# Optimization experiments

Hardware: AMD Instinct MI355X
Metric: run time of the kernel (lower is better)

Reference implementation:

```python
import jax, jax.numpy as jnp
import numpy as np

N_NODES = 50000
N_EDGES = 800000
HID = 128
EDGE_DIM = 4
LAYERS = 4
MAX_Z = 100
NUM_GRAPHS = 512


def setup_inputs() -> dict:
    key = jax.random.key(0)
    ks = jax.random.split(key, 16)
    s = lambda k, shape, fan_in: jax.random.normal(k, shape, jnp.float32) / np.sqrt(fan_in)
    inp = {
        "z": jax.random.randint(ks[0], (N_NODES,), 0, MAX_Z + 1),
        "edge_index": jax.random.randint(ks[1], (2, N_EDGES), 0, N_NODES),
        "edge_attr": jax.random.normal(ks[2], (N_EDGES, EDGE_DIM), jnp.float32),
        "batch": jnp.sort(jax.random.randint(ks[3], (N_NODES,), 0, NUM_GRAPHS)),
        "emb": jax.random.normal(ks[4], (MAX_Z + 1, HID), jnp.float32),
        # stacked per-layer params; Linear stored as [in, out]
        "ew1": s(ks[5], (LAYERS, 2 * HID + EDGE_DIM, HID), 2 * HID + EDGE_DIM),
        "eb1": jnp.zeros((LAYERS, HID), jnp.float32),
        "ew2": s(ks[6], (LAYERS, HID, HID), HID),
        "eb2": jnp.zeros((LAYERS, HID), jnp.float32),
        "nw": s(ks[7], (LAYERS, 2 * HID, HID), 2 * HID),
        "nb": jnp.zeros((LAYERS, HID), jnp.float32),
        "rw1": s(ks[8], (HID, HID), HID),
        "rb1": jnp.zeros((HID,), jnp.float32),
        "rw2": s(ks[9], (HID, 1), HID),
        "rb2": jnp.zeros((1,), jnp.float32),
    }
    return inp


def _forward(z, edge_index, edge_attr, batch,
             emb, ew1, eb1, ew2, eb2, nw, nb, rw1, rb1, rw2, rb2):
    silu = jax.nn.silu
    src, dst = edge_index[0], edge_index[1]
    x = emb[z]  # [N, H]
    for l in range(LAYERS):
        m_in = jnp.concatenate([x[src], x[dst], edge_attr], axis=-1)  # [E, 2H+ed]
        h = silu(m_in @ ew1[l] + eb1[l])
        msg = silu(h @ ew2[l] + eb2[l])  # [E, H]
        agg = jax.ops.segment_sum(msg, dst, num_segments=N_NODES)  # scatter-add
        x = silu(jnp.concatenate([x, agg], axis=-1) @ nw[l] + nb[l])
    # segment mean over graphs
    sums = jax.ops.segment_sum(x, batch, num_segments=NUM_GRAPHS)
    counts = jnp.clip(jax.ops.segment_sum(jnp.ones((x.shape[0],), x.dtype), batch,
                                          num_segments=NUM_GRAPHS), 1.0)[:, None]
    g = sums / counts  # [G, H]
    pred = (silu(g @ rw1 + rb1) @ rw2 + rb2)[:, 0]  # [G]
    return pred


def reference(z, edge_index, edge_attr, batch,
              emb, ew1, eb1, ew2, eb2, nw, nb, rw1, rb1, rw2, rb2):
    return _forward(z, edge_index, edge_attr, batch,
                    emb, ew1, eb1, ew2, eb2, nw, nb, rw1, rb1, rw2, rb2)
```

## Files before the change

### kernel.cpp

```cpp
#include <hip/hip_runtime.h>
#include <math.h>

#define HID  128
#define EDIM 4

typedef unsigned short u16;
typedef u16    us8   __attribute__((ext_vector_type(8)));
typedef __bf16 bf16x8 __attribute__((ext_vector_type(8)));
typedef float  f32x4 __attribute__((ext_vector_type(4)));

__device__ __forceinline__ float silu_f(float v) {
    return v * __builtin_amdgcn_rcpf(1.0f + __expf(-v));
}
__device__ __forceinline__ u16 f2bf(float f) {
    unsigned u = __float_as_uint(f);
    unsigned r = u + 0x7fffu + ((u >> 16) & 1u);
    return (u16)(r >> 16);
}
__device__ __forceinline__ u16 f2bf_fast(float f) {
    return (u16)((__float_as_uint(f) + 0x8000u) >> 16);
}
__device__ __forceinline__ float bf2f(u16 s) {
    return __uint_as_float(((unsigned)s) << 16);
}
__device__ __forceinline__ bf16x8 as_bf(us8 v) {
    return __builtin_bit_cast(bf16x8, v);
}

__device__ __forceinline__ void wfrag_one(const float* __restrict__ w,
        u16* __restrict__ out, int KT, int K, int idx) {
    int lane = idx & 63;
    int f    = (idx >> 6) % (KT * 8);
    int l    = idx / (64 * KT * 8);
    int kt = f >> 3, nt = f & 7;
    int n  = nt * 16 + (lane & 15);
    int k0 = kt * 32 + ((lane >> 4) * 8);
    us8 v;
    #pragma unroll
    for (int j = 0; j < 8; ++j) {
        int k = k0 + j;
        v[j] = (k < K) ? f2bf(w[((size_t)l * K + k) * HID + n]) : (u16)0;
    }
    *(us8*)&out[((size_t)(l * KT * 8 + f) * 64 + lane) * 8] = v;
}

#define T1 (4 * 9 * 8 * 64)
#define T2 (4 * 4 * 8 * 64)
#define T3 (4 * 8 * 8 * 64)

__global__ __launch_bounds__(256) void setup_kernel(
        const float* __restrict__ ew1, const float* __restrict__ ew2,
        const float* __restrict__ nw,
        u16* __restrict__ w1f, u16* __restrict__ w2f, u16* __restrict__ nwf,
        int* __restrict__ cnt, int* __restrict__ cursor,
        float* __restrict__ sums, float* __restrict__ cnts_g, int N, int G) {
    int idx = blockIdx.x * 256 + threadIdx.x;
    if (idx < T1) { wfrag_one(ew1, w1f, 9, 2 * HID + EDIM, idx); return; }
    idx -= T1;
    if (idx < T2) { wfrag_one(ew2, w2f, 4, HID, idx); return; }
    idx -= T2;
    if (idx < T3) { wfrag_one(nw, nwf, 8, 2 * HID, idx); return; }
    idx -= T3;
    if (idx < N) { cnt[idx] = 0; return; }
    idx -= N;
    if (idx < N) { cursor[idx] = 0; return; }
    idx -= N;
    if (idx < G * HID) { sums[idx] = 0.f; return; }
    idx -= G * HID;
    if (idx < G) { cnts_g[idx] = 0.f; return; }
}

__global__ __launch_bounds__(256) void hist_kernel(const int* __restrict__ dst,
        int* __restrict__ cnt, int E) {
    int e = blockIdx.x * 256 + threadIdx.x;
    if (e < E) atomicAdd(&cnt[dst[e]], 1);
}

__global__ __launch_bounds__(1024) void scan_kernel(const int* __restrict__ cnt,
        int* __restrict__ rowptr, int n) {
    __shared__ int s[1024];
    const int t = threadIdx.x;
    const int chunk = (n + 1023) >> 10;
    int lo = t * chunk, hi = lo + chunk;
    if (lo > n) lo = n;
    if (hi > n) hi = n;
    int sum = 0;
    for (int i = lo; i < hi; ++i) sum += cnt[i];
    s[t] = sum;
    __syncthreads();
    for (int off = 1; off < 1024; off <<= 1) {
        int v = (t >= off) ? s[t - off] : 0;
        __syncthreads();
        s[t] += v;
        __syncthreads();
    }
    int run = s[t] - sum;
    for (int i = lo; i < hi; ++i) { rowptr[i] = run; run += cnt[i]; }
    if (t == 1023) rowptr[n] = run;
}

__global__ __launch_bounds__(256) void scatter_kernel(const int* __restrict__ src,
        const int* __restrict__ dst, const float* __restrict__ ea,
        const int* __restrict__ rowptr, int* __restrict__ cursor,
        int* __restrict__ srcS, int* __restrict__ dstS, u16* __restrict__ eaS, int E) {
    int e = blockIdx.x * 256 + threadIdx.x;
    if (e >= E) return;
    int d = dst[e];
    int p = rowptr[d] + atomicAdd(&cursor[d], 1);
    srcS[p] = src[e];
    dstS[p] = d;
    const float* q = &ea[(size_t)e * EDIM];
    ushort4 v;
    v.x = f2bf(q[0]); v.y = f2bf(q[1]); v.z = f2bf(q[2]); v.w = f2bf(q[3]);
    *(ushort4*)&eaS[(size_t)p * 4] = v;
}

__global__ __launch_bounds__(HID) void embed_kernel(const int* __restrict__ z,
        const float* __restrict__ emb, u16* __restrict__ xb,
        float* __restrict__ agg, const int* __restrict__ batch,
        float* __restrict__ counts, int n) {
    int i = blockIdx.x;
    if (i >= n) return;
    int t = threadIdx.x;
    xb[(size_t)i * HID + t] = f2bf(emb[(size_t)z[i] * HID + t]);
    agg[(size_t)i * HID + t] = 0.f;
    if (t == 0) unsafeAtomicAdd(&counts[batch[i]], 1.0f);
}

__global__ __launch_bounds__(256) void edge_mfma(
        const u16* __restrict__ xin, const int* __restrict__ srcS,
        const int* __restrict__ dstS, const u16* __restrict__ eaS,
        const u16* __restrict__ w1f, const float* __restrict__ b1,
        const u16* __restrict__ w2f, const float* __restrict__ b2,
        float* __restrict__ agg, int nE) {
    __shared__ __align__(16) char smem[64 * 296 * 2];
    __shared__ int dsh[64];
    u16*   A = (u16*)smem;
    u16*   H = (u16*)smem;
    float* M = (float*)smem;

    const int t    = threadIdx.x;
    const int e0   = blockIdx.x * 64;
    const int wv   = t >> 6, lane = t & 63;
    const int lrow = lane & 15;
    const int kq   = lane >> 4;
    const int kq8  = kq * 8;
    const int rq   = kq * 4;

    #pragma unroll
    for (int it = 0; it < 8; ++it) {
        int slot = it * 256 + t;
        int row = slot >> 5, ch = slot & 31;
        int e = e0 + row; if (e >= nE) e = nE - 1;
        int node = (ch < 16) ? srcS[e] : dstS[e];
        us8 v = *(const us8*)&xin[(size_t)node * HID + (ch & 15) * 8];
        *(us8*)&A[row * 296 + ch * 8] = v;
    }
    if (t < 64) {
        int e = e0 + t;
        bool valid = e < nE; if (!valid) e = nE - 1;
        dsh[t] = valid ? dstS[e] : -1;
        ushort4 q = *(const ushort4*)&eaS[(size_t)e * 4];
        int base = t * 296 + 256;
        A[base + 0] = q.x; A[base + 1] = q.y; A[base + 2] = q.z; A[base + 3] = q.w;
        #pragma unroll
        for (int j = 4; j < 32; ++j) A[base + j] = 0;
    }
    __syncthreads();

    f32x4 acc[4][2];
    {
        float bias0 = b1[wv * 32 + lrow], bias1 = b1[wv * 32 + 16 + lrow];
        #pragma unroll
        for (int mt = 0; mt < 4; ++mt)
            #pragma unroll
            for (int r = 0; r < 4; ++r) {
                acc[mt][0][r] = bias0; acc[mt][1][r] = bias1;
            }
    }
    #pragma unroll
    for (int kt = 0; kt < 9; ++kt) {
        bf16x8 w0 = *(const bf16x8*)&w1f[((size_t)(kt * 8 + wv * 2 + 0) * 64 + lane) * 8];
        bf16x8 w1 = *(const bf16x8*)&w1f[((size_t)(kt * 8 + wv * 2 + 1) * 64 + lane) * 8];
        #pragma unroll
        for (int mt = 0; mt < 4; ++mt) {
            bf16x8 a = *(const bf16x8*)&A[(mt * 16 + lrow) * 296 + kt * 32 + kq8];
            acc[mt][0] = __builtin_amdgcn_mfma_f32_16x16x32_bf16(a, w0, acc[mt][0], 0, 0, 0);
            acc[mt][1] = __builtin_amdgcn_mfma_f32_16x16x32_bf16(a, w1, acc[mt][1], 0, 0, 0);
        }
    }
    __syncthreads();

    #pragma unroll
    for (int mt = 0; mt < 4; ++mt)
        #pragma unroll
        for (int nt2 = 0; nt2 < 2; ++nt2)
            #pragma unroll
            for (int r = 0; r < 4; ++r)
                H[(mt * 16 + rq + r) * 136 + wv * 32 + nt2 * 16 + lrow] =
                    f2bf_fast(silu_f(acc[mt][nt2][r]));
    __syncthreads();

    f32x4 acc2[4][2];
    {
        float bias0 = b2[wv * 32 + lrow], bias1 = b2[wv * 32 + 16 + lrow];
        #pragma unroll
        for (int mt = 0; mt < 4; ++mt)
            #pragma unroll
            for (int r = 0; r < 4; ++r) {
                acc2[mt][0][r] = bias0; acc2[mt][1][r] = bias1;
            }
    }
    #pragma unroll
    for (int kt = 0; kt < 4; ++kt) {
        bf16x8 w0 = *(const bf16x8*)&w2f[((size_t)(kt * 8 + wv * 2 + 0) * 64 + lane) * 8];
        bf16x8 w1 = *(const bf16x8*)&w2f[((size_t)(kt * 8 + wv * 2 + 1) * 64 + lane) * 8];
        #pragma unroll
        for (int mt = 0; mt < 4; ++mt) {
            bf16x8 a = *(const bf16x8*)&H[(mt * 16 + lrow) * 136 + kt * 32 + kq8];
            acc2[mt][0] = __builtin_amdgcn_mfma_f32_16x16x32_bf16(a, w0, acc2[mt][0], 0, 0, 0);
            acc2[mt][1] = __builtin_amdgcn_mfma_f32_16x16x32_bf16(a, w1, acc2[mt][1], 0, 0, 0);
        }
    }
    __syncthreads();

    #pragma unroll
    for (int mt = 0; mt < 4; ++mt)
        #pragma unroll
        for (int nt2 = 0; nt2 < 2; ++nt2)
            #pragma unroll
            for (int r = 0; r < 4; ++r)
                M[(mt * 16 + rq + r) * 132 + wv * 32 + nt2 * 16 + lrow] =
                    silu_f(acc2[mt][nt2][r]);

    {
        int col = wv * 32 + (lane & 31);
        int r0  = (lane >> 5) * 32;
        float run = 0.f;
        int   cur = dsh[r0];
        #pragma unroll 4
        for (int i = 0; i < 32; ++i) {
            int row = r0 + i;
            run += M[row * 132 + col];
            int nxt = (i == 31) ? -2 : dsh[row + 1];
            if (cur != nxt) {
                if (cur >= 0)
                    unsafeAtomicAdd(&agg[(size_t)cur * HID + col], run);
                run = 0.f; cur = nxt;
            }
        }
    }
}

__global__ __launch_bounds__(256) void node_mfma(
        u16* __restrict__ xb, float* __restrict__ agg,
        const u16* __restrict__ nwf, const float* __restrict__ nb,
        const int* __restrict__ batch, float* __restrict__ sums,
        int last, int n) {
    const int t    = threadIdx.x;
    const int i0   = blockIdx.x * 32;
    const int wv   = t >> 6, lane = t & 63;
    const int lrow = lane & 15;
    const int kq   = lane >> 4;
    const int kq8  = kq * 8;
    const int rq   = kq * 4;

    int iN[2];
    #pragma unroll
    for (int mt = 0; mt < 2; ++mt) {
        int i = i0 + mt * 16 + lrow; if (i >= n) i = n - 1;
        iN[mt] = i;
    }

    f32x4 acc[2][2];
    {
        float bias0 = nb[wv * 32 + lrow], bias1 = nb[wv * 32 + 16 + lrow];
        #pragma unroll
        for (int mt = 0; mt < 2; ++mt)
            #pragma unroll
            for (int r = 0; r < 4; ++r) {
                acc[mt][0][r] = bias0; acc[mt][1][r] = bias1;
            }
    }
    #pragma unroll
    for (int kt = 0; kt < 4; ++kt) {
        bf16x8 w0 = *(const bf16x8*)&nwf[((size_t)(kt * 8 + wv * 2 + 0) * 64 + lane) * 8];
        bf16x8 w1 = *(const bf16x8*)&nwf[((size_t)(kt * 8 + wv * 2 + 1) * 64 + lane) * 8];
        #pragma unroll
        for (int mt = 0; mt < 2; ++mt) {
            bf16x8 a = as_bf(*(const us8*)&xb[(size_t)iN[mt] * HID + kt * 32 + kq8]);
            acc[mt][0] = __builtin_amdgcn_mfma_f32_16x16x32_bf16(a, w0, acc[mt][0], 0, 0, 0);
            acc[mt][1] = __builtin_amdgcn_mfma_f32_16x16x32_bf16(a, w1, acc[mt][1], 0, 0, 0);
        }
    }
    #pragma unroll
    for (int kt = 4; kt < 8; ++kt) {
        bf16x8 w0 = *(const bf16x8*)&nwf[((size_t)(kt * 8 + wv * 2 + 0) * 64 + lane) * 8];
        bf16x8 w1 = *(const bf16x8*)&nwf[((size_t)(kt * 8 + wv * 2 + 1) * 64 + lane) * 8];
        #pragma unroll
        for (int mt = 0; mt < 2; ++mt) {
            const float* p = &agg[(size_t)iN[mt] * HID + (kt - 4) * 32 + kq8];
            float4 f0 = *(const float4*)p;
            float4 f1 = *(const float4*)(p + 4);
            us8 av;
            av[0] = f2bf_fast(f0.x); av[1] = f2bf_fast(f0.y);
            av[2] = f2bf_fast(f0.z); av[3] = f2bf_fast(f0.w);
            av[4] = f2bf_fast(f1.x); av[5] = f2bf_fast(f1.y);
            av[6] = f2bf_fast(f1.z); av[7] = f2bf_fast(f1.w);
            bf16x8 a = as_bf(av);
            acc[mt][0] = __builtin_amdgcn_mfma_f32_16x16x32_bf16(a, w0, acc[mt][0], 0, 0, 0);
            acc[mt][1] = __builtin_amdgcn_mfma_f32_16x16x32_bf16(a, w1, acc[mt][1], 0, 0, 0);
        }
    }

    if (!last) {
        __syncthreads();
        const float4 z4 = make_float4(0.f, 0.f, 0.f, 0.f);
        #pragma unroll
        for (int kt = 0; kt < 4; ++kt)
            #pragma unroll
            for (int mt = 0; mt < 2; ++mt) {
                float* p = &agg[(size_t)iN[mt] * HID + kt * 32 + kq8];
                *(float4*)p = z4; *(float4*)(p + 4) = z4;
            }
        #pragma unroll
        for (int mt = 0; mt < 2; ++mt)
            #pragma unroll
            for (int nt2 = 0; nt2 < 2; ++nt2)
                #pragma unroll
                for (int r = 0; r < 4; ++r) {
                    int i = i0 + mt * 16 + rq + r;
                    if (i < n)
                        xb[(size_t)i * HID + wv * 32 + nt2 * 16 + lrow] =
                            f2bf_fast(silu_f(acc[mt][nt2][r]));
                }
    } else {
        #pragma unroll
        for (int mt = 0; mt < 2; ++mt)
            #pragma unroll
            for (int nt2 = 0; nt2 < 2; ++nt2)
                #pragma unroll
                for (int r = 0; r < 4; ++r) {
                    int i = i0 + mt * 16 + rq + r;
                    if (i < n) {
                        int b = batch[i];
                        unsafeAtomicAdd(&sums[(size_t)b * HID + wv * 32 + nt2 * 16 + lrow],
                                        silu_f(acc[mt][nt2][r]));
                    }
                }
    }
}

__global__ __launch_bounds__(HID) void readout_kernel(
        const float* __restrict__ sums, const float* __restrict__ counts,
        const float* __restrict__ rw1, const float* __restrict__ rb1,
        const float* __restrict__ rw2, const float* __restrict__ rb2,
        float* __restrict__ pred) {
    __shared__ float gv[HID];
    __shared__ float hv[HID];
    const int g = blockIdx.x;
    const int t = threadIdx.x;
    float c = counts[g];
    if (c < 1.0f) c = 1.0f;
    gv[t] = sums[(size_t)g * HID + t] / c;
    __syncthreads();
    float acc = rb1[t];
    for (int k4 = 0; k4 < 32; ++k4) {
        float4 mv = *(const float4*)&gv[k4 * 4];
        #pragma unroll
        for (int j = 0; j < 4; ++j)
            acc += ((const float*)&mv)[j] * rw1[(size_t)(k4 * 4 + j) * HID + t];
    }
    hv[t] = silu_f(acc) * rw2[t];
    __syncthreads();
    for (int s = HID / 2; s > 0; s >>= 1) {
        if (t < s) hv[t] += hv[t + s];
        __syncthreads();
    }
    if (t == 0) pred[g] = hv[0] + rb2[0];
}

extern "C" void kernel_launch(void* const* d_in, const int* in_sizes, int n_in,
                              void* d_out, int out_size, void* d_ws, size_t ws_size,
                              hipStream_t stream) {
    const int*   z          = (const int*)d_in[0];
    const int*   edge_index = (const int*)d_in[1];
    const float* edge_attr  = (const float*)d_in[2];
    const int*   batch      = (const int*)d_in[3];
    const float* emb        = (const float*)d_in[4];
    const float* ew1        = (const float*)d_in[5];
    const float* eb1        = (const float*)d_in[6];
    const float* ew2        = (const float*)d_in[7];
    const float* eb2        = (const float*)d_in[8];
    const float* nw         = (const float*)d_in[9];
    const float* nb         = (const float*)d_in[10];
    const float* rw1        = (const float*)d_in[11];
    const float* rb1        = (const float*)d_in[12];
    const float* rw2        = (const float*)d_in[13];
    const float* rb2        = (const float*)d_in[14];
    float* pred = (float*)d_out;

    const int N = in_sizes[0];
    const int E = in_sizes[1] / 2;
    const int G = out_size;
    const int* srcI = edge_index;
    const int* dstI = edge_index + E;

    char* base = (char*)d_ws;
    size_t off = 0;
    auto carve = [&](size_t bytes) -> char* {
        char* p = base + off;
        off = (off + bytes + 255) & ~(size_t)255;
        return p;
    };
    float* agg    = (float*)carve((size_t)N * HID * sizeof(float));
    float* sums   = (float*)carve((size_t)G * HID * sizeof(float));
    float* cnts_g = (float*)carve((size_t)G * sizeof(float));
    u16*   xb     = (u16*)carve((size_t)N * HID * sizeof(u16));
    int*   srcS   = (int*)carve((size_t)(E + 64) * sizeof(int));
    int*   dstS   = (int*)carve((size_t)(E + 64) * sizeof(int));
    u16*   eaS    = (u16*)carve((size_t)(E + 64) * 4 * sizeof(u16));
    int*   rowptr = (int*)carve((size_t)(N + 1) * sizeof(int));
    int*   cursor = (int*)carve((size_t)N * sizeof(int));
    int*   cnt    = (int*)carve((size_t)N * sizeof(int));
    u16*   w1f    = (u16*)carve((size_t)4 * 72 * 512 * sizeof(u16));
    u16*   w2f    = (u16*)carve((size_t)4 * 32 * 512 * sizeof(u16));
    u16*   nwf    = (u16*)carve((size_t)4 * 64 * 512 * sizeof(u16));

    {
        long long total = (long long)T1 + T2 + T3 + 2LL * N + (long long)G * HID + G;
        int blocks = (int)((total + 255) / 256);
        setup_kernel<<<blocks, 256, 0, stream>>>(ew1, ew2, nw, w1f, w2f, nwf,
                                                 cnt, cursor, sums, cnts_g, N, G);
    }

    hist_kernel<<<(E + 255) / 256, 256, 0, stream>>>(dstI, cnt, E);
    scan_kernel<<<1, 1024, 0, stream>>>(cnt, rowptr, N);
    scatter_kernel<<<(E + 255) / 256, 256, 0, stream>>>(
        srcI, dstI, edge_attr, rowptr, cursor, srcS, dstS, eaS, E);

    embed_kernel<<<N, HID, 0, stream>>>(z, emb, xb, agg, batch, cnts_g, N);

    for (int l = 0; l < 4; ++l) {
        edge_mfma<<<(E + 63) / 64, 256, 0, stream>>>(
            xb, srcS, dstS, eaS,
            w1f + (size_t)l * 72 * 512, eb1 + (size_t)l * HID,
            w2f + (size_t)l * 32 * 512, eb2 + (size_t)l * HID,
            agg, E);
        node_mfma<<<(N + 31) / 32, 256, 0, stream>>>(
            xb, agg, nwf + (size_t)l * 64 * 512, nb + (size_t)l * HID,
            batch, sums, (l == 3) ? 1 : 0, N);
    }

    readout_kernel<<<G, HID, 0, stream>>>(sums, cnts_g, rw1, rb1, rw2, rb2, pred);
}
```

Measured before the change: 1.112 ms.

## Split edge MLP tile across 8 waves and swap MFMA operands for vector stores

The edge kernel now runs 512 threads per 64-edge block. Eight waves split the tile into two row halves by four column quarters, so each wave keeps half as many accumulators. MFMA operands are swapped so each lane's results are contiguous along the hidden dimension, which lets H and M be written with packed 8-byte and 16-byte LDS stores instead of scalar ones. The per-block segmented reduction is split into 16-row runs. This may issue more atomics at run boundaries, and the doubled wave count relies on the register budget fitting the new launch bounds.

```diff
diff --git a/kernel.cpp b/kernel.cpp
--- a/kernel.cpp
+++ b/kernel.cpp
@@ -19,6 +19,10 @@
 }
 __device__ __forceinline__ u16 f2bf_fast(float f) {
     return (u16)((__float_as_uint(f) + 0x8000u) >> 16);
+}
+__device__ __forceinline__ unsigned pack_bf2(float a, float b) {
+    return ((__float_as_uint(a) + 0x8000u) >> 16) |
+           ((__float_as_uint(b) + 0x8000u) & 0xffff0000u);
 }
 __device__ __forceinline__ float bf2f(u16 s) {
     return __uint_as_float(((unsigned)s) << 16);
@@ -127,7 +131,7 @@
     if (t == 0) unsafeAtomicAdd(&counts[batch[i]], 1.0f);
 }
 
-__global__ __launch_bounds__(256) void edge_mfma(
+__global__ __launch_bounds__(512, 8) void edge_mfma(
         const u16* __restrict__ xin, const int* __restrict__ srcS,
         const int* __restrict__ dstS, const u16* __restrict__ eaS,
         const u16* __restrict__ w1f, const float* __restrict__ b1,
@@ -146,10 +150,12 @@
     const int kq   = lane >> 4;
     const int kq8  = kq * 8;
     const int rq   = kq * 4;
-
-    #pragma unroll
-    for (int it = 0; it < 8; ++it) {
-        int slot = it * 256 + t;
+    const int h    = wv >> 2;
+    const int p    = wv & 3;
+
+    #pragma unroll
+    for (int it = 0; it < 4; ++it) {
+        int slot = it * 512 + t;
         int row = slot >> 5, ch = slot & 31;
         int e = e0 + row; if (e >= nE) e = nE - 1;
         int node = (ch < 16) ? srcS[e] : dstS[e];
@@ -168,81 +174,77 @@
     }
     __syncthreads();
 
-    f32x4 acc[4][2];
+    f32x4 acc[2][2];
+    #pragma unroll
+    for (int nt = 0; nt < 2; ++nt) {
+        f32x4 bv = *(const f32x4*)&b1[(p * 2 + nt) * 16 + rq];
+        acc[0][nt] = bv; acc[1][nt] = bv;
+    }
+    #pragma unroll
+    for (int kt = 0; kt < 9; ++kt) {
+        bf16x8 w0 = *(const bf16x8*)&w1f[((size_t)(kt * 8 + p * 2 + 0) * 64 + lane) * 8];
+        bf16x8 w1 = *(const bf16x8*)&w1f[((size_t)(kt * 8 + p * 2 + 1) * 64 + lane) * 8];
+        #pragma unroll
+        for (int mt = 0; mt < 2; ++mt) {
+            bf16x8 a = *(const bf16x8*)&A[((h * 2 + mt) * 16 + lrow) * 296 + kt * 32 + kq8];
+            acc[mt][0] = __builtin_amdgcn_mfma_f32_16x16x32_bf16(w0, a, acc[mt][0], 0, 0, 0);
+            acc[mt][1] = __builtin_amdgcn_mfma_f32_16x16x32_bf16(w1, a, acc[mt][1], 0, 0, 0);
+        }
+    }
+    __syncthreads();
+
+    #pragma unroll
+    for (int mt = 0; mt < 2; ++mt)
+        #pragma unroll
+        for (int nt = 0; nt < 2; ++nt) {
+            uint2 hv;
+            hv.x = pack_bf2(silu_f(acc[mt][nt][0]), silu_f(acc[mt][nt][1]));
+            hv.y = pack_bf2(silu_f(acc[mt][nt][2]), silu_f(acc[mt][nt][3]));
+            int edge = (h * 2 + mt) * 16 + lrow;
+            *(uint2*)&H[edge * 136 + (p * 2 + nt) * 16 + rq] = hv;
+        }
+    __syncthreads();
+
+    f32x4 acc2[2][2];
+    #pragma unroll
+    for (int nt = 0; nt < 2; ++nt) {
+        f32x4 bv = *(const f32x4*)&b2[(p * 2 + nt) * 16 + rq];
+        acc2[0][nt] = bv; acc2[1][nt] = bv;
+    }
+    #pragma unroll
+    for (int kt = 0; kt < 4; ++kt) {
+        bf16x8 w0 = *(const bf16x8*)&w2f[((size_t)(kt * 8 + p * 2 + 0) * 64 + lane) * 8];
+        bf16x8 w1 = *(const bf16x8*)&w2f[((size_t)(kt * 8 + p * 2 + 1) * 64 + lane) * 8];
+        #pragma unroll
+        for (int mt = 0; mt < 2; ++mt) {
+            bf16x8 a = *(const bf16x8*)&H[((h * 2 + mt) * 16 + lrow) * 136 + kt * 32 + kq8];
+            acc2[mt][0] = __builtin_amdgcn_mfma_f32_16x16x32_bf16(w0, a, acc2[mt][0], 0, 0, 0);
+            acc2[mt][1] = __builtin_amdgcn_mfma_f32_16x16x32_bf16(w1, a, acc2[mt][1], 0, 0, 0);
+        }
+    }
+    __syncthreads();
+
+    #pragma unroll
+    for (int mt = 0; mt < 2; ++mt)
+        #pragma unroll
+        for (int nt = 0; nt < 2; ++nt) {
+            f32x4 mv;
+            #pragma unroll
+            for (int r = 0; r < 4; ++r) mv[r] = silu_f(acc2[mt][nt][r]);
+            int edge = (h * 2 + mt) * 16 + lrow;
+            *(f32x4*)&M[edge * 132 + (p * 2 + nt) * 16 + rq] = mv;
+        }
+
     {
-        float bias0 = b1[wv * 32 + lrow], bias1 = b1[wv * 32 + 16 + lrow];
-        #pragma unroll
-        for (int mt = 0; mt < 4; ++mt)
-            #pragma unroll
-            for (int r = 0; r < 4; ++r) {
-                acc[mt][0][r] = bias0; acc[mt][1][r] = bias1;
-            }
-    }
-    #pragma unroll
-    for (int kt = 0; kt < 9; ++kt) {
-        bf16x8 w0 = *(const bf16x8*)&w1f[((size_t)(kt * 8 + wv * 2 + 0) * 64 + lane) * 8];
-        bf16x8 w1 = *(const bf16x8*)&w1f[((size_t)(kt * 8 + wv * 2 + 1) * 64 + lane) * 8];
-        #pragma unroll
-        for (int mt = 0; mt < 4; ++mt) {
-            bf16x8 a = *(const bf16x8*)&A[(mt * 16 + lrow) * 296 + kt * 32 + kq8];
-            acc[mt][0] = __builtin_amdgcn_mfma_f32_16x16x32_bf16(a, w0, acc[mt][0], 0, 0, 0);
-            acc[mt][1] = __builtin_amdgcn_mfma_f32_16x16x32_bf16(a, w1, acc[mt][1], 0, 0, 0);
-        }
-    }
-    __syncthreads();
-
-    #pragma unroll
-    for (int mt = 0; mt < 4; ++mt)
-        #pragma unroll
-        for (int nt2 = 0; nt2 < 2; ++nt2)
-            #pragma unroll
-            for (int r = 0; r < 4; ++r)
-                H[(mt * 16 + rq + r) * 136 + wv * 32 + nt2 * 16 + lrow] =
-                    f2bf_fast(silu_f(acc[mt][nt2][r]));
-    __syncthreads();
-
-    f32x4 acc2[4][2];
-    {
-        float bias0 = b2[wv * 32 + lrow], bias1 = b2[wv * 32 + 16 + lrow];
-        #pragma unroll
-        for (int mt = 0; mt < 4; ++mt)
-            #pragma unroll
-            for (int r = 0; r < 4; ++r) {
-                acc2[mt][0][r] = bias0; acc2[mt][1][r] = bias1;
-            }
-    }
-    #pragma unroll
-    for (int kt = 0; kt < 4; ++kt) {
-        bf16x8 w0 = *(const bf16x8*)&w2f[((size_t)(kt * 8 + wv * 2 + 0) * 64 + lane) * 8];
-        bf16x8 w1 = *(const bf16x8*)&w2f[((size_t)(kt * 8 + wv * 2 + 1) * 64 + lane) * 8];
-        #pragma unroll
-        for (int mt = 0; mt < 4; ++mt) {
-            bf16x8 a = *(const bf16x8*)&H[(mt * 16 + lrow) * 136 + kt * 32 + kq8];
-            acc2[mt][0] = __builtin_amdgcn_mfma_f32_16x16x32_bf16(a, w0, acc2[mt][0], 0, 0, 0);
-            acc2[mt][1] = __builtin_amdgcn_mfma_f32_16x16x32_bf16(a, w1, acc2[mt][1], 0, 0, 0);
-        }
-    }
-    __syncthreads();
-
-    #pragma unroll
-    for (int mt = 0; mt < 4; ++mt)
-        #pragma unroll
-        for (int nt2 = 0; nt2 < 2; ++nt2)
-            #pragma unroll
-            for (int r = 0; r < 4; ++r)
-                M[(mt * 16 + rq + r) * 132 + wv * 32 + nt2 * 16 + lrow] =
-                    silu_f(acc2[mt][nt2][r]);
-
-    {
-        int col = wv * 32 + (lane & 31);
-        int r0  = (lane >> 5) * 32;
+        int col = p * 32 + (lane & 31);
+        int r0  = h * 32 + (lane >> 5) * 16;
         float run = 0.f;
         int   cur = dsh[r0];
         #pragma unroll 4
-        for (int i = 0; i < 32; ++i) {
+        for (int i = 0; i < 16; ++i) {
             int row = r0 + i;
             run += M[row * 132 + col];
-            int nxt = (i == 31) ? -2 : dsh[row + 1];
+            int nxt = (i == 15) ? -2 : dsh[row + 1];
             if (cur != nxt) {
                 if (cur >= 0)
                     unsafeAtomicAdd(&agg[(size_t)cur * HID + col], run);
@@ -442,7 +444,7 @@
     embed_kernel<<<N, HID, 0, stream>>>(z, emb, xb, agg, batch, cnts_g, N);
 
     for (int l = 0; l < 4; ++l) {
-        edge_mfma<<<(E + 63) / 64, 256, 0, stream>>>(
+        edge_mfma<<<(E + 63) / 64, 512, 0, stream>>>(
             xb, srcS, dstS, eaS,
             w1f + (size_t)l * 72 * 512, eb1 + (size_t)l * HID,
             w2f + (size_t)l * 32 * 512, eb2 + (size_t)l * HID,
```

Measured after the change: 1.125 ms. No clear change (+1.2%).
